# Kernel tuning notes

Hardware: AMD Instinct MI355X
Metric: run time of the kernel (lower is better)

The kernel has to match this reference:

```python
import jax, jax.numpy as jnp
import numpy as np

N_QUBITS = 4
N_LAYERS = 2
BATCH = 524288


def _apply_1q(state, U, wire, batched):
    """Apply a 2x2 gate U on `wire`. state: [B,2,2,2,2]; U: [B,2,2] if batched else [2,2]."""
    ax = wire + 1
    s = jnp.moveaxis(state, ax, 1)
    if batched:
        s = jnp.einsum('bij,bj...->bi...', U, s)
    else:
        s = jnp.einsum('ij,bj...->bi...', U, s)
    return jnp.moveaxis(s, 1, ax)


def _apply_cnot(state, control, target):
    cax, tax = control + 1, target + 1
    s0 = jnp.take(state, 0, axis=cax)
    s1 = jnp.take(state, 1, axis=cax)
    t_ax = tax - 1 if tax > cax else tax  # target axis after removing control axis
    s1 = jnp.flip(s1, axis=t_ax)
    return jnp.stack([s0, s1], axis=cax)


def _circuit(x, weight):
    B = x.shape[0]
    # Angle encoding: RY(tanh(x_i) * pi) per wire (per-sample angles)
    theta = jnp.tanh(x) * jnp.pi  # [B, 4]
    state = jnp.zeros((B,) + (2,) * N_QUBITS, jnp.complex64)
    state = state.at[(slice(None),) + (0,) * N_QUBITS].set(1.0)
    for q in range(N_QUBITS):
        h = theta[:, q] * 0.5
        c, s = jnp.cos(h), jnp.sin(h)
        Ury = jnp.stack([jnp.stack([c, -s], -1), jnp.stack([s, c], -1)], -2).astype(jnp.complex64)  # [B,2,2]
        state = _apply_1q(state, Ury, q, batched=True)
    for layer in range(N_LAYERS):
        for q in range(N_QUBITS):
            hy = weight[layer, q, 0] * 0.5
            cy, sy = jnp.cos(hy), jnp.sin(hy)
            Uy = jnp.stack([jnp.stack([cy, -sy]), jnp.stack([sy, cy])]).astype(jnp.complex64)
            state = _apply_1q(state, Uy, q, batched=False)
            hz = weight[layer, q, 1] * 0.5
            ez = jnp.exp(-1j * hz.astype(jnp.complex64))
            z0 = jnp.zeros((), jnp.complex64)
            Uz = jnp.stack([jnp.stack([ez, z0]), jnp.stack([z0, jnp.conj(ez)])])
            state = _apply_1q(state, Uz, q, batched=False)
        for q in range(N_QUBITS):
            state = _apply_cnot(state, q, (q + 1) % N_QUBITS)
    # <Z_i> = P(bit_i = 0) - P(bit_i = 1)
    probs = jnp.abs(state) ** 2  # [B,2,2,2,2] float32
    outs = []
    for q in range(N_QUBITS):
        other_axes = tuple(a for a in range(1, N_QUBITS + 1) if a != q + 1)
        marg = probs.sum(other_axes)  # [B,2]
        outs.append(marg[:, 0] - marg[:, 1])
    return jnp.stack(outs, axis=-1).astype(jnp.float32)  # [B,4]


def setup_inputs() -> dict:
    key = jax.random.key(0)
    kx, kw = jax.random.split(key)
    x = jax.random.normal(kx, (BATCH, N_QUBITS), dtype=jnp.float32)
    weight = jax.random.normal(kw, (N_LAYERS, N_QUBITS, 2), dtype=jnp.float32) * 0.1
    return {"x": x, "weight": weight}


def reference(x, weight):
    return _circuit(x, weight)
```

## Files before the change

### kernel.cpp

```cpp
#include <hip/hip_runtime.h>
#include <math.h>


#define HALF_PI_F 1.57079632679489661923f

__global__ __launch_bounds__(256) void qlayer_kernel(
    const float* __restrict__ x,
    const float* __restrict__ weight,
    float* __restrict__ out,
    int B)
{
    __shared__ float cw[16], sw[16];
    if (threadIdx.x < 16) {
        float h = 0.5f * weight[threadIdx.x];
        __sincosf(h, &sw[threadIdx.x], &cw[threadIdx.x]);
    }
    __syncthreads();

    int tid = blockIdx.x * blockDim.x + threadIdx.x;
    if (tid >= B) return;

    float4 xv = reinterpret_cast<const float4*>(x)[tid];

    float c[4], s[4];
    {
        float xs[4] = {xv.x, xv.y, xv.z, xv.w};
        #pragma unroll
        for (int q = 0; q < 4; ++q) {
            float t = tanhf(xs[q]);
            __sincosf(t * HALF_PI_F, &s[q], &c[q]);
        }
    }

    float re[16], im[16];
    {
        float p01[4] = {c[0]*c[1], c[0]*s[1], s[0]*c[1], s[0]*s[1]};
        float p23[4] = {c[2]*c[3], c[2]*s[3], s[2]*c[3], s[2]*s[3]};
        #pragma unroll
        for (int a = 0; a < 4; ++a)
            #pragma unroll
            for (int b = 0; b < 4; ++b) {
                re[a*4+b] = p01[a]*p23[b];
                im[a*4+b] = 0.0f;
            }
    }

    #pragma unroll
    for (int layer = 0; layer < 2; ++layer) {
        #pragma unroll
        for (int q = 0; q < 4; ++q) {
            float cy = cw[layer*8 + q*2 + 0];
            float sy = sw[layer*8 + q*2 + 0];
            float cz = cw[layer*8 + q*2 + 1];
            float sz = sw[layer*8 + q*2 + 1];
            int st = 8 >> q;
            #pragma unroll
            for (int i = 0; i < 16; ++i) {
                if (i & st) continue;
                int j = i | st;
                float r0 = re[i], r1 = re[j], i0 = im[i], i1 = im[j];
                float nr0 = cy*r0 - sy*r1;
                float nr1 = sy*r0 + cy*r1;
                float ni0 = cy*i0 - sy*i1;
                float ni1 = sy*i0 + cy*i1;
                re[i] = nr0*cz + ni0*sz;
                im[i] = ni0*cz - nr0*sz;
                re[j] = nr1*cz - ni1*sz;
                im[j] = ni1*cz + nr1*sz;
            }
        }
        #pragma unroll
        for (int q = 0; q < 4; ++q) {
            int cb = 8 >> q;
            int tb = 8 >> ((q + 1) & 3);
            #pragma unroll
            for (int i = 0; i < 16; ++i) {
                if ((i & cb) && !(i & tb)) {
                    int j = i | tb;
                    float tr = re[i]; re[i] = re[j]; re[j] = tr;
                    float ti = im[i]; im[i] = im[j]; im[j] = ti;
                }
            }
        }
    }

    float p[16];
    #pragma unroll
    for (int i = 0; i < 16; ++i) p[i] = re[i]*re[i] + im[i]*im[i];

    float z[4] = {0.f, 0.f, 0.f, 0.f};
    #pragma unroll
    for (int i = 0; i < 16; ++i) {
        #pragma unroll
        for (int q = 0; q < 4; ++q)
            z[q] += (i & (8 >> q)) ? -p[i] : p[i];
    }

    float4 o = {z[0], z[1], z[2], z[3]};
    reinterpret_cast<float4*>(out)[tid] = o;
}

extern "C" void kernel_launch(void* const* d_in, const int* in_sizes, int n_in,
                              void* d_out, int out_size, void* d_ws, size_t ws_size,
                              hipStream_t stream) {
    const float* x = (const float*)d_in[0];
    const float* w = (const float*)d_in[1];
    float* out = (float*)d_out;
    int B = in_sizes[0] / 4;
    int block = 256;
    int grid = (B + block - 1) / block;
    qlayer_kernel<<<grid, block, 0, stream>>>(x, w, out, B);
}
```

Before: 76.72 us.

## Precompute circuit unitary observable as quadratic form, evaluate per-sample via symmetric contraction

A single-block prologue kernel builds the fixed 16x16 circuit unitary from the weights and folds each Z observable into a symmetric 400-entry coefficient table in workspace. The main kernel then only computes the product-state amplitudes and contracts them against the table with fused multiply-adds, replacing the per-sample gate simulation. tanh is also replaced with an exp-based fast approximation. This adds a second launch with a dependency, and the per-sample kernel now reads the coefficient table from global memory (likely cached), which may cost slightly in accuracy from the fast math.

```diff
diff --git a/kernel.cpp b/kernel.cpp
--- a/kernel.cpp
+++ b/kernel.cpp
@@ -4,96 +4,143 @@
 
 #define HALF_PI_F 1.57079632679489661923f
 
-__global__ __launch_bounds__(256) void qlayer_kernel(
-    const float* __restrict__ x,
+__global__ __launch_bounds__(256) void build_C(
     const float* __restrict__ weight,
-    float* __restrict__ out,
-    int B)
+    float* __restrict__ C)
 {
     __shared__ float cw[16], sw[16];
+    __shared__ float Ur[16][16], Ui[16][16];
+    __shared__ float A[4][16][16];
+
     if (threadIdx.x < 16) {
         float h = 0.5f * weight[threadIdx.x];
         __sincosf(h, &sw[threadIdx.x], &cw[threadIdx.x]);
     }
     __syncthreads();
 
+    if (threadIdx.x < 16) {
+        int col = threadIdx.x;
+        float re[16], im[16];
+        #pragma unroll
+        for (int i = 0; i < 16; ++i) { re[i] = 0.f; im[i] = 0.f; }
+        re[col] = 1.f;
+
+        #pragma unroll
+        for (int layer = 0; layer < 2; ++layer) {
+            #pragma unroll
+            for (int q = 0; q < 4; ++q) {
+                float cy = cw[layer*8 + q*2 + 0];
+                float sy = sw[layer*8 + q*2 + 0];
+                float cz = cw[layer*8 + q*2 + 1];
+                float sz = sw[layer*8 + q*2 + 1];
+                int st = 8 >> q;
+                #pragma unroll
+                for (int i = 0; i < 16; ++i) {
+                    if (i & st) continue;
+                    int j = i | st;
+                    float r0 = re[i], r1 = re[j], i0 = im[i], i1 = im[j];
+                    float nr0 = cy*r0 - sy*r1;
+                    float nr1 = sy*r0 + cy*r1;
+                    float ni0 = cy*i0 - sy*i1;
+                    float ni1 = sy*i0 + cy*i1;
+                    re[i] = nr0*cz + ni0*sz;
+                    im[i] = ni0*cz - nr0*sz;
+                    re[j] = nr1*cz - ni1*sz;
+                    im[j] = ni1*cz + nr1*sz;
+                }
+            }
+            #pragma unroll
+            for (int q = 0; q < 4; ++q) {
+                int cb = 8 >> q;
+                int tb = 8 >> ((q + 1) & 3);
+                #pragma unroll
+                for (int i = 0; i < 16; ++i) {
+                    if ((i & cb) && !(i & tb)) {
+                        int j = i | tb;
+                        float tr = re[i]; re[i] = re[j]; re[j] = tr;
+                        float ti = im[i]; im[i] = im[j]; im[j] = ti;
+                    }
+                }
+            }
+        }
+        #pragma unroll
+        for (int i = 0; i < 16; ++i) { Ur[i][col] = re[i]; Ui[i][col] = im[i]; }
+    }
+    __syncthreads();
+
+    for (int e = threadIdx.x; e < 1024; e += 256) {
+        int q = e >> 8, j = (e >> 4) & 15, k = e & 15;
+        float sum = 0.f;
+        for (int i = 0; i < 16; ++i) {
+            float t = Ur[i][j]*Ur[i][k] + Ui[i][j]*Ui[i][k];
+            sum += (i & (8 >> q)) ? -t : t;
+        }
+        A[q][j][k] = sum;
+    }
+    __syncthreads();
+
+    for (int e = threadIdx.x; e < 400; e += 256) {
+        int q = e / 100, pi = (e / 10) % 10, qi = e % 10;
+        const int pu[10] = {0,0,0,0,1,1,1,2,2,3};
+        const int pv[10] = {0,1,2,3,1,2,3,2,3,3};
+        int u = pu[pi], v = pv[pi], r = pu[qi], s = pv[qi];
+        float sum = 0.f;
+        int a1s[2] = {u, v}, a2s[2] = {v, u};
+        int b1s[2] = {r, s}, b2s[2] = {s, r};
+        int na = (u == v) ? 1 : 2;
+        int nb = (r == s) ? 1 : 2;
+        for (int ia = 0; ia < na; ++ia)
+            for (int ib = 0; ib < nb; ++ib)
+                sum += A[q][a1s[ia]*4 + b1s[ib]][a2s[ia]*4 + b2s[ib]];
+        C[e] = sum;
+    }
+}
+
+__global__ __launch_bounds__(256) void qmain(
+    const float* __restrict__ x,
+    const float* __restrict__ C,
+    float* __restrict__ out,
+    int B)
+{
     int tid = blockIdx.x * blockDim.x + threadIdx.x;
     if (tid >= B) return;
 
     float4 xv = reinterpret_cast<const float4*>(x)[tid];
+    float xs[4] = {xv.x, xv.y, xv.z, xv.w};
 
     float c[4], s[4];
-    {
-        float xs[4] = {xv.x, xv.y, xv.z, xv.w};
-        #pragma unroll
-        for (int q = 0; q < 4; ++q) {
-            float t = tanhf(xs[q]);
-            __sincosf(t * HALF_PI_F, &s[q], &c[q]);
-        }
+    #pragma unroll
+    for (int q = 0; q < 4; ++q) {
+        float e = __expf(2.f * xs[q]);
+        float t = 1.f - __fdividef(2.f, e + 1.f);
+        __sincosf(t * HALF_PI_F, &s[q], &c[q]);
     }
 
-    float re[16], im[16];
-    {
-        float p01[4] = {c[0]*c[1], c[0]*s[1], s[0]*c[1], s[0]*s[1]};
-        float p23[4] = {c[2]*c[3], c[2]*s[3], s[2]*c[3], s[2]*s[3]};
-        #pragma unroll
-        for (int a = 0; a < 4; ++a)
-            #pragma unroll
-            for (int b = 0; b < 4; ++b) {
-                re[a*4+b] = p01[a]*p23[b];
-                im[a*4+b] = 0.0f;
-            }
+    float a4[4] = {c[0]*c[1], c[0]*s[1], s[0]*c[1], s[0]*s[1]};
+    float b4[4] = {c[2]*c[3], c[2]*s[3], s[2]*c[3], s[2]*s[3]};
+
+    const int pu[10] = {0,0,0,0,1,1,1,2,2,3};
+    const int pv[10] = {0,1,2,3,1,2,3,2,3,3};
+    float P[10], Q[10];
+    #pragma unroll
+    for (int i2 = 0; i2 < 10; ++i2) {
+        P[i2] = a4[pu[i2]] * a4[pv[i2]];
+        Q[i2] = b4[pu[i2]] * b4[pv[i2]];
     }
 
+    float z[4];
     #pragma unroll
-    for (int layer = 0; layer < 2; ++layer) {
+    for (int q = 0; q < 4; ++q) {
+        float zq = 0.f;
         #pragma unroll
-        for (int q = 0; q < 4; ++q) {
-            float cy = cw[layer*8 + q*2 + 0];
-            float sy = sw[layer*8 + q*2 + 0];
-            float cz = cw[layer*8 + q*2 + 1];
-            float sz = sw[layer*8 + q*2 + 1];
-            int st = 8 >> q;
+        for (int pi = 0; pi < 10; ++pi) {
+            float t = 0.f;
             #pragma unroll
-            for (int i = 0; i < 16; ++i) {
-                if (i & st) continue;
-                int j = i | st;
-                float r0 = re[i], r1 = re[j], i0 = im[i], i1 = im[j];
-                float nr0 = cy*r0 - sy*r1;
-                float nr1 = sy*r0 + cy*r1;
-                float ni0 = cy*i0 - sy*i1;
-                float ni1 = sy*i0 + cy*i1;
-                re[i] = nr0*cz + ni0*sz;
-                im[i] = ni0*cz - nr0*sz;
-                re[j] = nr1*cz - ni1*sz;
-                im[j] = ni1*cz + nr1*sz;
-            }
+            for (int qi = 0; qi < 10; ++qi)
+                t = fmaf(C[q*100 + pi*10 + qi], Q[qi], t);
+            zq = fmaf(P[pi], t, zq);
         }
-        #pragma unroll
-        for (int q = 0; q < 4; ++q) {
-            int cb = 8 >> q;
-            int tb = 8 >> ((q + 1) & 3);
-            #pragma unroll
-            for (int i = 0; i < 16; ++i) {
-                if ((i & cb) && !(i & tb)) {
-                    int j = i | tb;
-                    float tr = re[i]; re[i] = re[j]; re[j] = tr;
-                    float ti = im[i]; im[i] = im[j]; im[j] = ti;
-                }
-            }
-        }
-    }
-
-    float p[16];
-    #pragma unroll
-    for (int i = 0; i < 16; ++i) p[i] = re[i]*re[i] + im[i]*im[i];
-
-    float z[4] = {0.f, 0.f, 0.f, 0.f};
-    #pragma unroll
-    for (int i = 0; i < 16; ++i) {
-        #pragma unroll
-        for (int q = 0; q < 4; ++q)
-            z[q] += (i & (8 >> q)) ? -p[i] : p[i];
+        z[q] = zq;
     }
 
     float4 o = {z[0], z[1], z[2], z[3]};
@@ -106,8 +153,11 @@
     const float* x = (const float*)d_in[0];
     const float* w = (const float*)d_in[1];
     float* out = (float*)d_out;
+    float* C = (float*)d_ws;
     int B = in_sizes[0] / 4;
+
+    build_C<<<1, 256, 0, stream>>>(w, C);
     int block = 256;
     int grid = (B + block - 1) / block;
-    qlayer_kernel<<<grid, block, 0, stream>>>(x, w, out, B);
+    qmain<<<grid, block, 0, stream>>>(x, C, out, B);
 }
```

After: 73.79 us. 1.04x faster.
